# Kernel tuning notes

Hardware: AMD Instinct MI355X
Metric: run time of the kernel (lower is better)

## Reference

```python
import jax, jax.numpy as jnp
import numpy as np
import math

B, S = 4, 1024
V, D, L, H, F, MAXLEN = 32000, 1024, 6, 16, 4096, 2048
DH = D // H
NUM_BUCKETS, MAX_DIST = 32, 256
REL_SCALE = 64.0 ** 0.5
EPS = 1e-5


def setup_inputs() -> dict:
    key = jax.random.key(0)
    ks = iter(jax.random.split(key, 32))
    sd = 0.02
    inp = {
        'src': jax.random.randint(next(ks), (B, S), 0, V),
        'src_mask': jnp.ones((B, 1, 1, S), dtype=jnp.int32),
        'tok_emb': jax.random.normal(next(ks), (V, D), jnp.float32) * sd,
        'pos_emb': jax.random.normal(next(ks), (MAXLEN, D), jnp.float32) * sd,
        'Wq': jax.random.normal(next(ks), (L, D, D), jnp.float32) * sd,
        'bq': jnp.zeros((L, D), jnp.float32),
        'Wk': jax.random.normal(next(ks), (L, D, D), jnp.float32) * sd,
        'bk': jnp.zeros((L, D), jnp.float32),
        'Wv': jax.random.normal(next(ks), (L, D, D), jnp.float32) * sd,
        'bv': jnp.zeros((L, D), jnp.float32),
        'Wo': jax.random.normal(next(ks), (L, D, D), jnp.float32) * sd,
        'bo': jnp.zeros((L, D), jnp.float32),
        'rel_bias': jax.random.normal(next(ks), (L, NUM_BUCKETS, H), jnp.float32) * sd,
        'ln1_g': jnp.ones((L, D), jnp.float32),
        'ln1_b': jnp.zeros((L, D), jnp.float32),
        'W1': jax.random.normal(next(ks), (L, D, F), jnp.float32) * sd,
        'b1': jnp.zeros((L, F), jnp.float32),
        'W2': jax.random.normal(next(ks), (L, F, D), jnp.float32) * sd,
        'b2': jnp.zeros((L, D), jnp.float32),
        'ln2_g': jnp.ones((L, D), jnp.float32),
        'ln2_b': jnp.zeros((L, D), jnp.float32),
    }
    return inp


def _rel_pos_bucket(seq_len):
    # non-causal bucketing (T5-style), matching the torch source
    q = jnp.arange(seq_len)
    k = jnp.arange(seq_len)
    n = q[:, None] - k[None, :]          # == -(k - q)
    nb = NUM_BUCKETS // 2                # 16
    ret = (n < 0).astype(jnp.int32) * nb
    n = jnp.abs(n)
    max_exact = nb // 2                  # 8
    is_small = n < max_exact
    val_large = max_exact + (
        jnp.log(jnp.maximum(n, 1).astype(jnp.float32) / max_exact)
        / math.log(MAX_DIST / max_exact) * (nb - max_exact)
    ).astype(jnp.int32)
    val_large = jnp.minimum(val_large, nb - 1)
    return ret + jnp.where(is_small, n, val_large)  # [S,S] in [0,32)


def _layer_norm(x, g, b):
    mu = jnp.mean(x, axis=-1, keepdims=True)
    var = jnp.var(x, axis=-1, keepdims=True)
    return (x - mu) * jax.lax.rsqrt(var + EPS) * g + b


def reference(src, src_mask, tok_emb, pos_emb, Wq, bq, Wk, bk, Wv, bv, Wo, bo,
              rel_bias, ln1_g, ln1_b, W1, b1, W2, b2, ln2_g, ln2_b):
    seq_len = src.shape[1]
    bucket = _rel_pos_bucket(seq_len)                      # [S,S] int
    x = tok_emb[src] * jnp.sqrt(jnp.float32(D)) + pos_emb[jnp.arange(seq_len)][None]
    scale = jnp.sqrt(jnp.float32(DH))
    neg = jnp.float32(-1e10)

    def layer(x, p):
        (wq, bq_, wk, bk_, wv, bv_, wo, bo_, rb, g1, b1_, w1, bb1, w2, bb2, g2, b2_) = p
        Q = (x @ wq + bq_).reshape(B, seq_len, H, DH)
        K = (x @ wk + bk_).reshape(B, seq_len, H, DH)
        Vv = (x @ wv + bv_).reshape(B, seq_len, H, DH)
        energy = jnp.einsum('bqhd,bkhd->bhqk', Q, K) / scale
        energy = jnp.where(src_mask == 0, neg, energy)
        bias = rb[bucket]                                  # [S,S,H]
        energy = energy + jnp.transpose(bias, (2, 0, 1))[None] * REL_SCALE
        attn = jax.nn.softmax(energy, axis=-1)
        o = jnp.einsum('bhqk,bkhd->bqhd', attn, Vv).reshape(B, seq_len, D)
        o = o @ wo + bo_
        x = _layer_norm(x + o, g1, b1_)
        f = jax.nn.relu(x @ w1 + bb1) @ w2 + bb2
        x = _layer_norm(x + f, g2, b2_)
        return x, None

    params = (Wq, bq, Wk, bk, Wv, bv, Wo, bo, rel_bias,
              ln1_g, ln1_b, W1, b1, W2, b2, ln2_g, ln2_b)
    x, _ = jax.lax.scan(layer, x, params)
    return x
```

## Files before the change

kernel.cpp:

```cpp
#include <hip/hip_runtime.h>

#define B_ 4
#define S_ 1024
#define D_ 1024
#define F_ 4096
#define H_ 16
#define L_ 6
#define M_ (B_*S_)

#define LOG2E 1.44269504088896f

typedef unsigned short u16;
typedef __attribute__((ext_vector_type(4))) unsigned short u16x4;
typedef __attribute__((ext_vector_type(8))) short s16x8;
typedef __attribute__((ext_vector_type(8))) __bf16 bf16x8;
typedef __attribute__((ext_vector_type(4))) float f32x4;

typedef const __attribute__((address_space(1))) unsigned int gu32;
typedef __attribute__((address_space(3))) unsigned int su32;

__device__ __forceinline__ u16 f2bf(float f) {
  union { float f; unsigned u; } v; v.f = f;
  unsigned u = v.u;
  return (u16)((u + 0x7fffu + ((u >> 16) & 1u)) >> 16);
}
__device__ __forceinline__ float bf2f(u16 h) {
  union { unsigned u; float f; } v; v.u = (unsigned)h << 16; return v.f;
}

__device__ __forceinline__ f32x4 mfma16(s16x8 a, s16x8 b, f32x4 c) {
  return __builtin_amdgcn_mfma_f32_16x16x32_bf16(
      __builtin_bit_cast(bf16x8, a), __builtin_bit_cast(bf16x8, b), c, 0, 0, 0);
}

__device__ __forceinline__ void gload16(const void* g, void* s) {
  __builtin_amdgcn_global_load_lds((gu32*)g, (su32*)s, 16, 0, 0);
}

template<int OUTMODE>
__device__ __forceinline__ void gemm128_body(
    const u16* __restrict__ A, const u16* __restrict__ Bt,
    const float* __restrict__ b0, const float* __restrict__ b1,
    const float* __restrict__ b2, u16* __restrict__ Ch,
    int N, int K, int kbeg, int kend)
{
  __shared__ __align__(16) u16 As[128 * 64];
  __shared__ __align__(16) u16 Bs[128 * 64];
  const int tid = threadIdx.x, lane = tid & 63, w = tid >> 6;
  const int bm = blockIdx.x * 128, bn = blockIdx.y * 128;
  const int wm = (w >> 1) * 64, wn = (w & 1) * 64;

  f32x4 acc[4][4];
#pragma unroll
  for (int i = 0; i < 4; i++)
#pragma unroll
    for (int j = 0; j < 4; j++) acc[i][j] = {0.f, 0.f, 0.f, 0.f};

  for (int k0 = kbeg; k0 < kend; k0 += 64) {
    __syncthreads();
#pragma unroll
    for (int i = 0; i < 4; i++) {
      const int flat = i * 4096 + w * 1024 + lane * 16;
      const int row = flat >> 7, ce = (flat & 127) >> 1;
      gload16(A + (size_t)(bm + row) * K + k0 + ce, As + i * 2048 + w * 512);
      gload16(Bt + (size_t)(bn + row) * K + k0 + ce, Bs + i * 2048 + w * 512);
    }
    __syncthreads();
#pragma unroll
    for (int kk = 0; kk < 2; kk++) {
      s16x8 af[4], bf[4];
#pragma unroll
      for (int mf = 0; mf < 4; mf++)
        af[mf] = *(const s16x8*)&As[(wm + mf * 16 + (lane & 15)) * 64 + kk * 32 + (lane >> 4) * 8];
#pragma unroll
      for (int nf = 0; nf < 4; nf++)
        bf[nf] = *(const s16x8*)&Bs[(wn + nf * 16 + (lane & 15)) * 64 + kk * 32 + (lane >> 4) * 8];
#pragma unroll
      for (int mf = 0; mf < 4; mf++)
#pragma unroll
        for (int nf = 0; nf < 4; nf++)
          acc[mf][nf] = mfma16(af[mf], bf[nf], acc[mf][nf]);
    }
  }
#pragma unroll
  for (int nf = 0; nf < 4; nf++) {
    const int col = bn + wn + nf * 16 + (lane & 15);
    float bvv = 0.f, sc = 1.0f;
    int zz = 0, lc = col;
    if (OUTMODE == 3) {
      zz = col >> 10; lc = col & 1023;
      const float* bp = (zz == 0) ? b0 : (zz == 1) ? b1 : b2;
      bvv = bp[lc];
      sc = (zz == 0) ? (0.125f * LOG2E) : 1.0f;
    }
#pragma unroll
    for (int mf = 0; mf < 4; mf++) {
#pragma unroll
      for (int j = 0; j < 4; j++) {
        const int row = bm + wm + mf * 16 + ((lane >> 4) << 2) + j;
        const float v = acc[mf][nf][j];
        if (OUTMODE == 1) {
          Ch[(size_t)row * N + col] = f2bf(v);
        } else {
          Ch[(size_t)zz * M_ * D_ + (size_t)row * D_ + lc] = f2bf((v + bvv) * sc);
        }
      }
    }
  }
}

__global__ __launch_bounds__(256, 3) void gemm_qkvf(
    const u16* __restrict__ A, const u16* __restrict__ WT,
    const float* __restrict__ bq, const float* __restrict__ bk,
    const float* __restrict__ bv, u16* __restrict__ Out)
{
  gemm128_body<3>(A, WT, bq, bk, bv, Out, 3 * D_, D_, 0, D_);
}

__global__ __launch_bounds__(256, 3) void gemm_osplit2(
    const u16* __restrict__ A, const u16* __restrict__ WT,
    u16* __restrict__ P)
{
  const int z = blockIdx.z;
  gemm128_body<1>(A, WT, nullptr, nullptr, nullptr,
                  P + (size_t)z * M_ * D_, D_, D_, z * 512, z * 512 + 512);
}

__device__ __forceinline__ s16x8 readfrag(const u16* half, int r, int kk, int hi4) {
  const int c = (kk * 64 + hi4 * 16) ^ ((r & 7) << 4);
  return *(const s16x8*)((const char*)half + r * 128 + c);
}

__device__ __forceinline__ void stage_half(
    const u16* __restrict__ src, int ldk, u16* lds_half, int w, int lane)
{
#pragma unroll
  for (int j = 0; j < 2; j++) {
    const int flat = j * 8192 + w * 1024 + lane * 16;
    const int row = flat >> 7;
    const int kb = (flat & 127) ^ ((row & 7) << 4);
    gload16(src + (size_t)row * ldk + (kb >> 1), lds_half + j * 4096 + w * 512);
  }
}

#define BAR     asm volatile("s_barrier" ::: "memory")
#define PH_PRE  asm volatile("s_barrier" ::: "memory"); __builtin_amdgcn_s_setprio(1)
#define PH_POST __builtin_amdgcn_s_setprio(0); __builtin_amdgcn_sched_barrier(0)
#define VM4     asm volatile("s_waitcnt vmcnt(4)" ::: "memory")
#define VM0     asm volatile("s_waitcnt vmcnt(0)" ::: "memory")

#define READ_B(bufhalf) do { \
  _Pragma("unroll") for (int nf = 0; nf < 4; nf++) \
  _Pragma("unroll") for (int kk = 0; kk < 2; kk++) \
    bfr[nf][kk] = readfrag(bufhalf, rb0 + nf * 16 + lo16, kk, hi4); } while (0)
#define READ_A(bufhalf, Q) do { \
  _Pragma("unroll") for (int m = 0; m < 2; m++) \
  _Pragma("unroll") for (int kk = 0; kk < 2; kk++) \
    af[m][kk] = readfrag(bufhalf, (2 * (Q) + m) * 16 + lo16, kk, hi4); } while (0)
#define DO_MFMA(Q) do { \
  _Pragma("unroll") for (int kk = 0; kk < 2; kk++) \
  _Pragma("unroll") for (int m = 0; m < 2; m++) \
  _Pragma("unroll") for (int nf = 0; nf < 4; nf++) \
    acc[2 * (Q) + m][nf] = mfma16(af[m][kk], bfr[nf][kk], acc[2 * (Q) + m][nf]); } while (0)

template<int OUTMODE>
__device__ __forceinline__ void gemm256_body(
    const u16* __restrict__ A, const u16* __restrict__ Bt,
    const float* __restrict__ bias, u16* __restrict__ Ch,
    int N, int K, int kbeg, int kslice)
{
  __shared__ __align__(16) u16 As[2][2][8192];
  __shared__ __align__(16) u16 Bs[2][2][8192];
  const int tid = threadIdx.x, lane = tid & 63, w = tid >> 6;
  const int wr = w >> 2, wc = w & 3;
  const int lo16 = lane & 15, hi4 = lane >> 4;
  const int bm = blockIdx.x * 256, bn = blockIdx.y * 256;
  const int rb0 = (wc & 1) * 64;

  const u16* Abase = A + (size_t)bm * K + kbeg;
  const u16* Bbase = Bt + (size_t)bn * K + kbeg;
  const size_t h1 = (size_t)128 * K;
  const int NT = kslice >> 6, NI = NT >> 1;

  f32x4 acc[8][4];
#pragma unroll
  for (int i = 0; i < 8; i++)
#pragma unroll
    for (int j = 0; j < 4; j++) acc[i][j] = {0.f, 0.f, 0.f, 0.f};

  stage_half(Abase,           K, As[0][0], w, lane);
  stage_half(Abase + h1,      K, As[0][1], w, lane);
  stage_half(Bbase,           K, Bs[0][0], w, lane);
  stage_half(Bbase + h1,      K, Bs[0][1], w, lane);
  stage_half(Abase + 64,      K, As[1][0], w, lane);
  stage_half(Abase + h1 + 64, K, As[1][1], w, lane);
  stage_half(Bbase + 64,      K, Bs[1][0], w, lane);
  stage_half(Bbase + h1 + 64, K, Bs[1][1], w, lane);
  asm volatile("s_waitcnt vmcnt(8)" ::: "memory");
  BAR;

  const u16* Ae = As[0][wr]; const u16* Ao = As[1][wr];
  const u16* Be = Bs[0][wc >> 1]; const u16* Bo = Bs[1][wc >> 1];
  s16x8 af[2][2], bfr[4][2];

  for (int it = 0; it < NI - 1; ++it) {
    READ_B(Be); READ_A(Ae, 0);
    if (it > 0) {
      stage_half(Abase +      (size_t)(2 * it + 1) * 64, K, As[1][0], w, lane);
      stage_half(Abase + h1 + (size_t)(2 * it + 1) * 64, K, As[1][1], w, lane);
    }
    PH_PRE; DO_MFMA(0); PH_POST; BAR;
    READ_A(Ae, 1);
    stage_half(Bbase +      (size_t)(2 * it + 2) * 64, K, Bs[0][0], w, lane);
    PH_PRE; DO_MFMA(1); PH_POST; BAR;
    READ_A(Ae, 2);
    stage_half(Bbase + h1 + (size_t)(2 * it + 2) * 64, K, Bs[0][1], w, lane);
    PH_PRE; DO_MFMA(2); PH_POST; BAR;
    READ_A(Ae, 3);
    PH_PRE; DO_MFMA(3); PH_POST; VM4; BAR;
    READ_B(Bo); READ_A(Ao, 0);
    stage_half(Abase +      (size_t)(2 * it + 2) * 64, K, As[0][0], w, lane);
    stage_half(Abase + h1 + (size_t)(2 * it + 2) * 64, K, As[0][1], w, lane);
    PH_PRE; DO_MFMA(0); PH_POST; BAR;
    READ_A(Ao, 1);
    stage_half(Bbase +      (size_t)(2 * it + 3) * 64, K, Bs[1][0], w, lane);
    PH_PRE; DO_MFMA(1); PH_POST; BAR;
    READ_A(Ao, 2);
    stage_half(Bbase + h1 + (size_t)(2 * it + 3) * 64, K, Bs[1][1], w, lane);
    PH_PRE; DO_MFMA(2); PH_POST; BAR;
    READ_A(Ao, 3);
    PH_PRE; DO_MFMA(3); PH_POST; VM4; BAR;
  }
  READ_B(Be); READ_A(Ae, 0);
  stage_half(Abase +      (size_t)(NT - 1) * 64, K, As[1][0], w, lane);
  stage_half(Abase + h1 + (size_t)(NT - 1) * 64, K, As[1][1], w, lane);
  PH_PRE; DO_MFMA(0); PH_POST; BAR;
  READ_A(Ae, 1);             PH_PRE; DO_MFMA(1); PH_POST; BAR;
  READ_A(Ae, 2);             PH_PRE; DO_MFMA(2); PH_POST; BAR;
  READ_A(Ae, 3);             PH_PRE; DO_MFMA(3); PH_POST; VM0; BAR;
  READ_B(Bo); READ_A(Ao, 0); PH_PRE; DO_MFMA(0); PH_POST; BAR;
  READ_A(Ao, 1);             PH_PRE; DO_MFMA(1); PH_POST; BAR;
  READ_A(Ao, 2);             PH_PRE; DO_MFMA(2); PH_POST; BAR;
  READ_A(Ao, 3);             PH_PRE; DO_MFMA(3); PH_POST;

  const int row0 = bm + wr * 128, col0 = bn + wc * 64;
#pragma unroll
  for (int nf = 0; nf < 4; nf++) {
    const int col = col0 + nf * 16 + lo16;
    const float bv = (OUTMODE == 2) ? bias[col] : 0.f;
#pragma unroll
    for (int mf = 0; mf < 8; mf++) {
#pragma unroll
      for (int j = 0; j < 4; j++) {
        const int row = row0 + mf * 16 + hi4 * 4 + j;
        float v = acc[mf][nf][j];
        if (OUTMODE == 2) v = fmaxf(v + bv, 0.f);
        Ch[(size_t)row * N + col] = f2bf(v);
      }
    }
  }
}

__global__ __launch_bounds__(512, 2) void gemm_ffn1(
    const u16* __restrict__ A, const u16* __restrict__ WT,
    const float* __restrict__ bias, u16* __restrict__ Out)
{
  gemm256_body<2>(A, WT, bias, Out, F_, D_, 0, D_);
}

__global__ __launch_bounds__(512, 2) void gemm_ffn2sp4(
    const u16* __restrict__ A, const u16* __restrict__ WT,
    u16* __restrict__ P)
{
  const int z = blockIdx.z;
  gemm256_body<4>(A, WT, nullptr, P + (size_t)z * M_ * D_,
                  D_, F_, z * 1024, 1024);
}

__global__ __launch_bounds__(256) void transpose_all(
    const float* __restrict__ Wq, const float* __restrict__ Wk,
    const float* __restrict__ Wv, const float* __restrict__ Wo,
    const float* __restrict__ W1, const float* __restrict__ W2,
    u16* __restrict__ WTall)
{
  __shared__ float t[32][33];
  const int l = blockIdx.y;
  int bt = blockIdx.x;
  const float* src;
  u16* dst;
  int R, C, cx, cy;
  u16* base = WTall + (size_t)l * 12 * 1024 * 1024;
  if (bt < 4096) {
    const int m = bt >> 10; bt &= 1023;
    src = ((m == 0) ? Wq : (m == 1) ? Wk : (m == 2) ? Wv : Wo) + (size_t)l * D_ * D_;
    dst = base + (size_t)m * D_ * D_;
    R = D_; C = D_; cx = bt & 31; cy = bt >> 5;
  } else if (bt < 8192) {
    bt -= 4096;
    src = W1 + (size_t)l * D_ * F_;
    dst = base + 4 * 1024 * 1024;
    R = D_; C = F_; cx = bt & 127; cy = bt >> 7;
  } else {
    bt -= 8192;
    src = W2 + (size_t)l * D_ * F_;
    dst = base + 8 * 1024 * 1024;
    R = F_; C = D_; cx = bt & 31; cy = bt >> 5;
  }
  const int c0 = cx * 32, r0 = cy * 32;
  const int tx = threadIdx.x & 31, ty = threadIdx.x >> 5;
#pragma unroll
  for (int i = 0; i < 4; i++)
    t[ty + 8 * i][tx] = src[(size_t)(r0 + ty + 8 * i) * C + c0 + tx];
  __syncthreads();
#pragma unroll
  for (int i = 0; i < 4; i++)
    dst[(size_t)(c0 + ty + 8 * i) * R + r0 + tx] = f2bf(t[tx][ty + 8 * i]);
}

__global__ __launch_bounds__(256) void vt_transpose(
    const u16* __restrict__ Vb, u16* __restrict__ Vt)
{
  __shared__ u16 t[64][66];
  const int s0 = blockIdx.x * 64;
  const int bh = blockIdx.y;
  const int b = bh >> 4, h = bh & 15;
  const int tid = threadIdx.x;
  const int row = tid >> 2;
  const int c0 = (tid & 3) * 16;
  const u16* src = Vb + (size_t)(b * S_ + s0 + row) * D_ + h * 64 + c0;
  *(s16x8*)&t[row][c0] = *(const s16x8*)src;
  *(s16x8*)&t[row][c0 + 8] = *(const s16x8*)(src + 8);
  __syncthreads();
  const int dh = tid >> 2;
  const int sc = (tid & 3) * 16;
  s16x8 a, bv;
#pragma unroll
  for (int u = 0; u < 8; u++) a[u] = (short)t[sc + u][dh];
#pragma unroll
  for (int u = 0; u < 8; u++) bv[u] = (short)t[sc + 8 + u][dh];
  u16* dst = Vt + (size_t)(bh * 64 + dh) * S_ + s0 + sc;
  *(s16x8*)dst = a;
  *(s16x8*)(dst + 8) = bv;
}

__global__ __launch_bounds__(256) void build_lut(
    const float* __restrict__ rb, float* __restrict__ lut_g)
{
  const int h = blockIdx.x, l = blockIdx.y;
  for (int idx = threadIdx.x; idx < 2048; idx += 256) {
    const int rel = idx - 1024;
    const int ret = rel < 0 ? 16 : 0;
    const int n = rel < 0 ? -rel : rel;
    int bu;
    if (n < 8) bu = ret + n;
    else {
      const float t = logf((float)n * 0.125f) * (8.0f / 3.4657359027997265f);
      int vl = 8 + (int)t;
      if (vl > 15) vl = 15;
      bu = ret + vl;
    }
    lut_g[(size_t)(l * H_ + h) * 2048 + idx] = rb[l * 512 + bu * 16 + h] * (8.0f * LOG2E);
  }
}

__global__ __launch_bounds__(256) void mask2neg(
    const int* __restrict__ mask, u16* __restrict__ mf)
{
  const int i = blockIdx.x * 256 + threadIdx.x;
  if (i < B_ * S_) mf[i] = mask[i] ? (u16)0 : f2bf(-1e10f * LOG2E);
}

__device__ __forceinline__ s16x8 lds_swz(const u16* base, int row, int cb) {
  const int addr = row * 128 + (cb ^ ((row & 7) << 4));
  return *(const s16x8*)((const char*)base + addr);
}

#define ATTN_STAGE(t, buf) do { \
  const int kt2 = (t) * 64; \
  const int flat2 = tid * 16; \
  const int row2 = flat2 >> 7; \
  const int ce2 = ((flat2 & 127) ^ ((row2 & 7) << 4)) >> 1; \
  gload16(Kb + (size_t)(bS + kt2 + row2) * D_ + hh + ce2, Ks[buf] + w * 512); \
  gload16(Vt + (size_t)(bh * 64 + row2) * S_ + kt2 + ce2, Vs[buf] + w * 512); \
} while (0)

__global__ __launch_bounds__(512, 2) void attn_kernel(
    const u16* __restrict__ Qb, const u16* __restrict__ Kb,
    const u16* __restrict__ Vt, const u16* __restrict__ mask16,
    const float* __restrict__ lut_g, u16* __restrict__ AO)
{
  __shared__ __align__(16) float lut[2048];
  __shared__ __align__(16) u16 maskf[1024];
  __shared__ __align__(16) u16 Ks[2][64 * 64];
  __shared__ __align__(16) u16 Vs[2][64 * 64];
  __shared__ __align__(16) u16 Ps[8][16 * 68];

  const int tid = threadIdx.x;
  const int lane = tid & 63;
  const int w = tid >> 6;
  const int bh = blockIdx.x;
  const int b = bh >> 4, h = bh & 15;
  const int q0 = blockIdx.y * 128 + w * 16;
  const int bS = b * S_, hh = h * 64;
  const int lo16 = lane & 15, hi4 = lane >> 4;

  const float* lsrc = lut_g + (size_t)h * 2048;
  gload16(lsrc + w * 256 + lane * 4, lut + w * 256);
  if (w < 2)
    gload16(mask16 + bS + w * 512 + lane * 8, maskf + w * 512);

  s16x8 qf[2];
#pragma unroll
  for (int kk = 0; kk < 2; kk++)
    qf[kk] = *(const s16x8*)(Qb + (size_t)(bS + q0 + lo16) * D_ + hh +
                             kk * 32 + hi4 * 8);

  s16x8 onesf;
#pragma unroll
  for (int u = 0; u < 8; u++) onesf[u] = (short)((lo16 == 0) ? 0x3F80 : 0);

  f32x4 oacc[5];
#pragma unroll
  for (int i = 0; i < 5; i++) oacc[i] = {0.f, 0.f, 0.f, 0.f};

  ATTN_STAGE(0, 0);
  asm volatile("s_waitcnt vmcnt(0) lgkmcnt(0)" ::: "memory");
  __builtin_amdgcn_s_barrier();

  for (int t = 0; t < S_ / 64; ++t) {
    const int cur = t & 1;
    const int kt = t * 64;
    if (t < S_ / 64 - 1) ATTN_STAGE(t + 1, cur ^ 1);

    f32x4 sacc[4];
#pragma unroll
    for (int i = 0; i < 4; i++) sacc[i] = {0.f, 0.f, 0.f, 0.f};
#pragma unroll
    for (int kk = 0; kk < 2; kk++) {
      const int cb = kk * 64 + hi4 * 16;
#pragma unroll
      for (int nf = 0; nf < 4; nf++) {
        const s16x8 kb = lds_swz(Ks[cur], nf * 16 + lo16, cb);
        sacc[nf] = mfma16(qf[kk], kb, sacc[nf]);
      }
    }

    float kmf[4];
#pragma unroll
    for (int nf = 0; nf < 4; nf++)
      kmf[nf] = bf2f(maskf[kt + nf * 16 + lo16]);

    const int lidx0 = q0 + hi4 * 4 + 1024 - kt - lo16;
#pragma unroll
    for (int j = 0; j < 4; j++) {
      const int lrow = (hi4 << 2) + j;
#pragma unroll
      for (int nf = 0; nf < 4; nf++) {
        const float s = sacc[nf][j] + kmf[nf] + lut[lidx0 + j - nf * 16];
        Ps[w][lrow * 68 + nf * 16 + lo16] = f2bf(__builtin_amdgcn_exp2f(s));
      }
    }

#pragma unroll
    for (int kk = 0; kk < 2; kk++) {
      const s16x8 pa = *(const s16x8*)&Ps[w][lo16 * 68 + kk * 32 + hi4 * 8];
      const int cb = kk * 64 + hi4 * 16;
#pragma unroll
      for (int df = 0; df < 4; df++) {
        const s16x8 vb = lds_swz(Vs[cur], df * 16 + lo16, cb);
        oacc[df] = mfma16(pa, vb, oacc[df]);
      }
      oacc[4] = mfma16(pa, onesf, oacc[4]);
    }

    asm volatile("s_waitcnt vmcnt(0)" ::: "memory");
    __builtin_amdgcn_s_barrier();
  }

  float inv[4];
#pragma unroll
  for (int j = 0; j < 4; j++) {
    const float l = __shfl(oacc[4][j], lane & 48);
    inv[j] = 1.0f / l;
  }
#pragma unroll
  for (int df = 0; df < 4; df++)
#pragma unroll
    for (int j = 0; j < 4; j++) {
      const int qrow = q0 + (hi4 << 2) + j;
      AO[(size_t)(bS + qrow) * D_ + hh + df * 16 + lo16] =
          f2bf(oacc[df][j] * inv[j]);
    }
}

template<int NP>
__global__ __launch_bounds__(256) void ln_fusedb(
    const u16* __restrict__ Xh, const u16* __restrict__ P,
    const float* __restrict__ bias, const float* __restrict__ g,
    const float* __restrict__ be, u16* __restrict__ Yh, float* __restrict__ Yf)
{
  const int row = blockIdx.x;
  const int tid = threadIdx.x;
  const size_t off = (size_t)row * D_;
  const size_t ps = (size_t)M_ * D_;
  const u16x4 xv = ((const u16x4*)(Xh + off))[tid];
  float v[4];
#pragma unroll
  for (int q = 0; q < 4; q++) v[q] = bf2f(xv[q]);
#pragma unroll
  for (int p = 0; p < NP; p++) {
    const u16x4 pv = ((const u16x4*)(P + p * ps + off))[tid];
#pragma unroll
    for (int q = 0; q < 4; q++) v[q] += bf2f(pv[q]);
  }
  const float4 bb = ((const float4*)bias)[tid];
  v[0] += bb.x; v[1] += bb.y; v[2] += bb.z; v[3] += bb.w;

  float sum = v[0] + v[1] + v[2] + v[3];
  float ss = v[0] * v[0] + v[1] * v[1] + v[2] * v[2] + v[3] * v[3];
#pragma unroll
  for (int o = 1; o < 64; o <<= 1) {
    sum += __shfl_xor(sum, o);
    ss += __shfl_xor(ss, o);
  }
  __shared__ float s1[4], s2[4];
  if ((tid & 63) == 0) { s1[tid >> 6] = sum; s2[tid >> 6] = ss; }
  __syncthreads();
  sum = s1[0] + s1[1] + s1[2] + s1[3];
  ss = s2[0] + s2[1] + s2[2] + s2[3];
  const float mu = sum * (1.f / D_);
  const float var = ss * (1.f / D_) - mu * mu;
  const float rstd = rsqrtf(var + 1e-5f);
  const float4 gv = ((const float4*)g)[tid];
  const float4 bv = ((const float4*)be)[tid];
  float y[4];
  y[0] = (v[0] - mu) * rstd * gv.x + bv.x;
  y[1] = (v[1] - mu) * rstd * gv.y + bv.y;
  y[2] = (v[2] - mu) * rstd * gv.z + bv.z;
  y[3] = (v[3] - mu) * rstd * gv.w + bv.w;
  u16x4 hv;
  hv.x = f2bf(y[0]); hv.y = f2bf(y[1]); hv.z = f2bf(y[2]); hv.w = f2bf(y[3]);
  ((u16x4*)(Yh + off))[tid] = hv;
  if (Yf != nullptr) {
    float4 yf; yf.x = y[0]; yf.y = y[1]; yf.z = y[2]; yf.w = y[3];
    ((float4*)(Yf + off))[tid] = yf;
  }
}

__global__ __launch_bounds__(256) void embed_kernel(
    const int* __restrict__ src, const float* __restrict__ tok,
    const float* __restrict__ pos, u16* __restrict__ Xh)
{
  const int row = blockIdx.x;
  const int s = row & (S_ - 1);
  const int t = src[row];
  const int tid = threadIdx.x;
  const float4 tv = ((const float4*)(tok + (size_t)t * D_))[tid];
  const float4 pv = ((const float4*)(pos + (size_t)s * D_))[tid];
  u16x4 hv;
  hv.x = f2bf(tv.x * 32.f + pv.x);
  hv.y = f2bf(tv.y * 32.f + pv.y);
  hv.z = f2bf(tv.z * 32.f + pv.z);
  hv.w = f2bf(tv.w * 32.f + pv.w);
  ((u16x4*)(Xh + (size_t)row * D_))[tid] = hv;
}

extern "C" void kernel_launch(void* const* d_in, const int* in_sizes, int n_in,
                              void* d_out, int out_size, void* d_ws, size_t ws_size,
                              hipStream_t stream)
{
  const int* src = (const int*)d_in[0];
  const int* mask = (const int*)d_in[1];
  const float* tok_emb = (const float*)d_in[2];
  const float* pos_emb = (const float*)d_in[3];
  const float* Wq = (const float*)d_in[4];
  const float* bq = (const float*)d_in[5];
  const float* Wk = (const float*)d_in[6];
  const float* bk = (const float*)d_in[7];
  const float* Wv = (const float*)d_in[8];
  const float* bv = (const float*)d_in[9];
  const float* Wo = (const float*)d_in[10];
  const float* bo = (const float*)d_in[11];
  const float* rb = (const float*)d_in[12];
  const float* g1 = (const float*)d_in[13];
  const float* b1n = (const float*)d_in[14];
  const float* W1 = (const float*)d_in[15];
  const float* b1f = (const float*)d_in[16];
  const float* W2 = (const float*)d_in[17];
  const float* b2f = (const float*)d_in[18];
  const float* g2 = (const float*)d_in[19];
  const float* b2n = (const float*)d_in[20];
  float* out = (float*)d_out;

  char* ws = (char*)d_ws;
  const size_t MB = 1ull << 20;
  u16* xb16  = (u16*)(ws + 0);
  u16* Qb16  = (u16*)(ws + 8 * MB);
  u16* Kb16  = (u16*)(ws + 16 * MB);
  u16* Vb16  = (u16*)(ws + 24 * MB);
  u16* Vt16  = (u16*)(ws + 32 * MB);
  u16* AO16  = (u16*)(ws + 40 * MB);
  u16* Pp16  = (u16*)(ws + 48 * MB);
  u16* WTall = (u16*)(ws + 80 * MB);
  u16* Hb16  = (u16*)(ws + 8 * MB);
  float* lut_g  = (float*)(ws + 224 * MB);
  u16*   mask16 = (u16*)(ws + 224 * MB + 786432);

  embed_kernel<<<M_, 256, 0, stream>>>(src, tok_emb, pos_emb, xb16);
  build_lut<<<dim3(H_, L_), 256, 0, stream>>>(rb, lut_g);
  mask2neg<<<(B_ * S_ + 255) / 256, 256, 0, stream>>>(mask, mask16);
  transpose_all<<<dim3(12288, L_), 256, 0, stream>>>(
      Wq, Wk, Wv, Wo, W1, W2, WTall);

  for (int l = 0; l < L_; l++) {
    u16* WTqkv = WTall + (size_t)l * 12 * 1024 * 1024;
    u16* WTo   = WTqkv + 3 * 1024 * 1024;
    u16* WT1   = WTqkv + 4 * 1024 * 1024;
    u16* WT2   = WTqkv + 8 * 1024 * 1024;

    gemm_qkvf<<<dim3(M_ / 128, 3 * D_ / 128), 256, 0, stream>>>(
        xb16, WTqkv, bq + l * D_, bk + l * D_, bv + l * D_, Qb16);

    vt_transpose<<<dim3(S_ / 64, B_ * H_), 256, 0, stream>>>(Vb16, Vt16);

    attn_kernel<<<dim3(B_ * H_, S_ / 128), 512, 0, stream>>>(
        Qb16, Kb16, Vt16, mask16, lut_g + (size_t)l * H_ * 2048, AO16);

    gemm_osplit2<<<dim3(M_ / 128, D_ / 128, 2), 256, 0, stream>>>(
        AO16, WTo, Pp16);

    ln_fusedb<2><<<M_, 256, 0, stream>>>(
        xb16, Pp16, bo + l * D_, g1 + l * D_, b1n + l * D_, xb16, nullptr);

    gemm_ffn1<<<dim3(M_ / 256, F_ / 256), 512, 0, stream>>>(
        xb16, WT1, b1f + l * F_, Hb16);

    gemm_ffn2sp4<<<dim3(M_ / 256, D_ / 256, 4), 512, 0, stream>>>(
        Hb16, WT2, Pp16);

    ln_fusedb<4><<<M_, 256, 0, stream>>>(
        xb16, Pp16, b2f + l * D_, g2 + l * D_, b2n + l * D_, xb16,
        (l == L_ - 1) ? out : nullptr);
  }
}
```

Before: 1.350 ms.

## Fuse V transpose into QKV GEMM epilogue and transpose weights per layer

The QKV GEMM epilogue now writes V directly in the transposed per-head layout, so the separate vt_transpose kernel and its extra read/write pass over V go away. The one-shot transpose of all layers' weights is replaced by a per-layer transpose kernel that reuses a single bf16 weight buffer. That kernel uses 64x64 tiles with float4 loads and 16-byte stores. The per-layer version shrinks workspace use and may keep weights warmer in cache, at the cost of an extra launch per layer. The transposed V stores are 8-byte strided writes, which may coalesce less well.

Measured after the change: 1.239 ms. 1.09x faster.

```diff
diff --git a/kernel.cpp b/kernel.cpp
--- a/kernel.cpp
+++ b/kernel.cpp
@@ -42,7 +42,7 @@
     const u16* __restrict__ A, const u16* __restrict__ Bt,
     const float* __restrict__ b0, const float* __restrict__ b1,
     const float* __restrict__ b2, u16* __restrict__ Ch,
-    int N, int K, int kbeg, int kend)
+    u16* __restrict__ Vt, int N, int K, int kbeg, int kend)
 {
   __shared__ __align__(16) u16 As[128 * 64];
   __shared__ __align__(16) u16 Bs[128 * 64];
@@ -82,27 +82,55 @@
           acc[mf][nf] = mfma16(af[mf], bf[nf], acc[mf][nf]);
     }
   }
-#pragma unroll
-  for (int nf = 0; nf < 4; nf++) {
-    const int col = bn + wn + nf * 16 + (lane & 15);
-    float bvv = 0.f, sc = 1.0f;
-    int zz = 0, lc = col;
-    if (OUTMODE == 3) {
-      zz = col >> 10; lc = col & 1023;
-      const float* bp = (zz == 0) ? b0 : (zz == 1) ? b1 : b2;
-      bvv = bp[lc];
-      sc = (zz == 0) ? (0.125f * LOG2E) : 1.0f;
-    }
-#pragma unroll
-    for (int mf = 0; mf < 4; mf++) {
-#pragma unroll
-      for (int j = 0; j < 4; j++) {
-        const int row = bm + wm + mf * 16 + ((lane >> 4) << 2) + j;
-        const float v = acc[mf][nf][j];
-        if (OUTMODE == 1) {
-          Ch[(size_t)row * N + col] = f2bf(v);
-        } else {
-          Ch[(size_t)zz * M_ * D_ + (size_t)row * D_ + lc] = f2bf((v + bvv) * sc);
+
+  if (OUTMODE == 3) {
+    const int zz = bn >> 10;
+    const int lcb = (bn & 1023) + wn;
+    const float* bp = (zz == 0) ? b0 : (zz == 1) ? b1 : b2;
+    if (zz == 2) {
+      const int b = bm >> 10;
+#pragma unroll
+      for (int nf = 0; nf < 4; nf++) {
+        const int dh2 = lcb + nf * 16 + (lane & 15);
+        const int hq = dh2 >> 6, dh = dh2 & 63;
+        const float bv = bp[dh2];
+        u16* vrow = Vt + ((size_t)((b << 4) + hq) * 64 + dh) * S_;
+#pragma unroll
+        for (int mf = 0; mf < 4; mf++) {
+          const int s0 = (bm & 1023) + wm + mf * 16 + ((lane >> 4) << 2);
+          u16x4 hv;
+#pragma unroll
+          for (int j = 0; j < 4; j++) hv[j] = f2bf(acc[mf][nf][j] + bv);
+          *(u16x4*)(vrow + s0) = hv;
+        }
+      }
+    } else {
+      const float sc = (zz == 0) ? (0.125f * LOG2E) : 1.0f;
+      u16* Outz = Ch + (size_t)zz * M_ * D_;
+#pragma unroll
+      for (int nf = 0; nf < 4; nf++) {
+        const int col = lcb + nf * 16 + (lane & 15);
+        const float bv = bp[col];
+#pragma unroll
+        for (int mf = 0; mf < 4; mf++) {
+#pragma unroll
+          for (int j = 0; j < 4; j++) {
+            const int row = bm + wm + mf * 16 + ((lane >> 4) << 2) + j;
+            Outz[(size_t)row * D_ + col] = f2bf((acc[mf][nf][j] + bv) * sc);
+          }
+        }
+      }
+    }
+  } else {
+#pragma unroll
+    for (int nf = 0; nf < 4; nf++) {
+      const int col = bn + wn + nf * 16 + (lane & 15);
+#pragma unroll
+      for (int mf = 0; mf < 4; mf++) {
+#pragma unroll
+        for (int j = 0; j < 4; j++) {
+          const int row = bm + wm + mf * 16 + ((lane >> 4) << 2) + j;
+          Ch[(size_t)row * N + col] = f2bf(acc[mf][nf][j]);
         }
       }
     }
@@ -112,9 +140,9 @@
 __global__ __launch_bounds__(256, 3) void gemm_qkvf(
     const u16* __restrict__ A, const u16* __restrict__ WT,
     const float* __restrict__ bq, const float* __restrict__ bk,
-    const float* __restrict__ bv, u16* __restrict__ Out)
-{
-  gemm128_body<3>(A, WT, bq, bk, bv, Out, 3 * D_, D_, 0, D_);
+    const float* __restrict__ bv, u16* __restrict__ Out, u16* __restrict__ Vt)
+{
+  gemm128_body<3>(A, WT, bq, bk, bv, Out, Vt, 3 * D_, D_, 0, D_);
 }
 
 __global__ __launch_bounds__(256, 3) void gemm_osplit2(
@@ -123,7 +151,7 @@
 {
   const int z = blockIdx.z;
   gemm128_body<1>(A, WT, nullptr, nullptr, nullptr,
-                  P + (size_t)z * M_ * D_, D_, D_, z * 512, z * 512 + 512);
+                  P + (size_t)z * M_ * D_, nullptr, D_, D_, z * 512, z * 512 + 512);
 }
 
 __device__ __forceinline__ s16x8 readfrag(const u16* half, int r, int kk, int hi4) {
@@ -277,70 +305,52 @@
                   D_, F_, z * 1024, 1024);
 }
 
-__global__ __launch_bounds__(256) void transpose_all(
+__global__ __launch_bounds__(256) void transpose_layer(
     const float* __restrict__ Wq, const float* __restrict__ Wk,
     const float* __restrict__ Wv, const float* __restrict__ Wo,
     const float* __restrict__ W1, const float* __restrict__ W2,
-    u16* __restrict__ WTall)
-{
-  __shared__ float t[32][33];
-  const int l = blockIdx.y;
+    u16* __restrict__ WT)
+{
+  __shared__ float tl[64][65];
   int bt = blockIdx.x;
-  const float* src;
-  u16* dst;
-  int R, C, cx, cy;
-  u16* base = WTall + (size_t)l * 12 * 1024 * 1024;
-  if (bt < 4096) {
-    const int m = bt >> 10; bt &= 1023;
-    src = ((m == 0) ? Wq : (m == 1) ? Wk : (m == 2) ? Wv : Wo) + (size_t)l * D_ * D_;
-    dst = base + (size_t)m * D_ * D_;
-    R = D_; C = D_; cx = bt & 31; cy = bt >> 5;
-  } else if (bt < 8192) {
-    bt -= 4096;
-    src = W1 + (size_t)l * D_ * F_;
-    dst = base + 4 * 1024 * 1024;
-    R = D_; C = F_; cx = bt & 127; cy = bt >> 7;
+  const float* src; u16* dst; int Rsrc, Csrc, cx, cy;
+  if (bt < 1024) {
+    const int m = bt >> 8; const int t = bt & 255;
+    src = (m == 0) ? Wq : (m == 1) ? Wk : (m == 2) ? Wv : Wo;
+    dst = WT + (size_t)m * 1024 * 1024;
+    Rsrc = 1024; Csrc = 1024; cx = t & 15; cy = t >> 4;
+  } else if (bt < 2048) {
+    const int t = bt - 1024;
+    src = W1; dst = WT + (size_t)4 * 1024 * 1024;
+    Rsrc = 1024; Csrc = 4096; cx = t & 63; cy = t >> 6;
   } else {
-    bt -= 8192;
-    src = W2 + (size_t)l * D_ * F_;
-    dst = base + 8 * 1024 * 1024;
-    R = F_; C = D_; cx = bt & 31; cy = bt >> 5;
-  }
-  const int c0 = cx * 32, r0 = cy * 32;
-  const int tx = threadIdx.x & 31, ty = threadIdx.x >> 5;
-#pragma unroll
-  for (int i = 0; i < 4; i++)
-    t[ty + 8 * i][tx] = src[(size_t)(r0 + ty + 8 * i) * C + c0 + tx];
+    const int t = bt - 2048;
+    src = W2; dst = WT + (size_t)8 * 1024 * 1024;
+    Rsrc = 4096; Csrc = 1024; cx = t & 15; cy = t >> 4;
+  }
+  const int r0 = cy * 64, c0 = cx * 64;
+  const int tid = threadIdx.x;
+  const int rl = tid >> 2, q = tid & 3;
+  const float* sp = src + (size_t)(r0 + rl) * Csrc + c0 + q * 16;
+#pragma unroll
+  for (int i = 0; i < 4; i++) {
+    const float4 v = *(const float4*)(sp + i * 4);
+    tl[rl][q * 16 + i * 4 + 0] = v.x;
+    tl[rl][q * 16 + i * 4 + 1] = v.y;
+    tl[rl][q * 16 + i * 4 + 2] = v.z;
+    tl[rl][q * 16 + i * 4 + 3] = v.w;
+  }
   __syncthreads();
 #pragma unroll
-  for (int i = 0; i < 4; i++)
-    dst[(size_t)(c0 + ty + 8 * i) * R + r0 + tx] = f2bf(t[tx][ty + 8 * i]);
-}
-
-__global__ __launch_bounds__(256) void vt_transpose(
-    const u16* __restrict__ Vb, u16* __restrict__ Vt)
-{
-  __shared__ u16 t[64][66];
-  const int s0 = blockIdx.x * 64;
-  const int bh = blockIdx.y;
-  const int b = bh >> 4, h = bh & 15;
-  const int tid = threadIdx.x;
-  const int row = tid >> 2;
-  const int c0 = (tid & 3) * 16;
-  const u16* src = Vb + (size_t)(b * S_ + s0 + row) * D_ + h * 64 + c0;
-  *(s16x8*)&t[row][c0] = *(const s16x8*)src;
-  *(s16x8*)&t[row][c0 + 8] = *(const s16x8*)(src + 8);
-  __syncthreads();
-  const int dh = tid >> 2;
-  const int sc = (tid & 3) * 16;
-  s16x8 a, bv;
-#pragma unroll
-  for (int u = 0; u < 8; u++) a[u] = (short)t[sc + u][dh];
-#pragma unroll
-  for (int u = 0; u < 8; u++) bv[u] = (short)t[sc + 8 + u][dh];
-  u16* dst = Vt + (size_t)(bh * 64 + dh) * S_ + s0 + sc;
-  *(s16x8*)dst = a;
-  *(s16x8*)(dst + 8) = bv;
+  for (int it = 0; it < 2; it++) {
+    const int idx = tid + it * 256;
+    const int cl = idx >> 3, seg = idx & 7;
+    const int rw0 = seg * 8;
+    s16x8 v8;
+#pragma unroll
+    for (int u = 0; u < 8; u++) v8[u] = (short)f2bf(tl[rw0 + u][cl]);
+    *(s16x8*)(dst + (size_t)(c0 + cl) * Rsrc + r0 + rw0) = v8;
+  }
 }
 
 __global__ __launch_bounds__(256) void build_lut(
@@ -597,31 +607,32 @@
   u16* xb16  = (u16*)(ws + 0);
   u16* Qb16  = (u16*)(ws + 8 * MB);
   u16* Kb16  = (u16*)(ws + 16 * MB);
-  u16* Vb16  = (u16*)(ws + 24 * MB);
-  u16* Vt16  = (u16*)(ws + 32 * MB);
-  u16* AO16  = (u16*)(ws + 40 * MB);
-  u16* Pp16  = (u16*)(ws + 48 * MB);
-  u16* WTall = (u16*)(ws + 80 * MB);
+  u16* Vt16  = (u16*)(ws + 24 * MB);
+  u16* AO16  = (u16*)(ws + 32 * MB);
+  u16* Pp16  = (u16*)(ws + 40 * MB);
+  u16* WT    = (u16*)(ws + 72 * MB);
   u16* Hb16  = (u16*)(ws + 8 * MB);
-  float* lut_g  = (float*)(ws + 224 * MB);
-  u16*   mask16 = (u16*)(ws + 224 * MB + 786432);
+  float* lut_g  = (float*)(ws + 96 * MB);
+  u16*   mask16 = (u16*)(ws + 96 * MB + 786432);
+
+  u16* WTqkv = WT;
+  u16* WTo   = WT + (size_t)3 * 1024 * 1024;
+  u16* WT1   = WT + (size_t)4 * 1024 * 1024;
+  u16* WT2   = WT + (size_t)8 * 1024 * 1024;
 
   embed_kernel<<<M_, 256, 0, stream>>>(src, tok_emb, pos_emb, xb16);
   build_lut<<<dim3(H_, L_), 256, 0, stream>>>(rb, lut_g);
   mask2neg<<<(B_ * S_ + 255) / 256, 256, 0, stream>>>(mask, mask16);
-  transpose_all<<<dim3(12288, L_), 256, 0, stream>>>(
-      Wq, Wk, Wv, Wo, W1, W2, WTall);
 
   for (int l = 0; l < L_; l++) {
-    u16* WTqkv = WTall + (size_t)l * 12 * 1024 * 1024;
-    u16* WTo   = WTqkv + 3 * 1024 * 1024;
-    u16* WT1   = WTqkv + 4 * 1024 * 1024;
-    u16* WT2   = WTqkv + 8 * 1024 * 1024;
+    const size_t oDD = (size_t)l * D_ * D_;
+    const size_t oDF = (size_t)l * D_ * F_;
+
+    transpose_layer<<<3072, 256, 0, stream>>>(
+        Wq + oDD, Wk + oDD, Wv + oDD, Wo + oDD, W1 + oDF, W2 + oDF, WT);
 
     gemm_qkvf<<<dim3(M_ / 128, 3 * D_ / 128), 256, 0, stream>>>(
-        xb16, WTqkv, bq + l * D_, bk + l * D_, bv + l * D_, Qb16);
-
-    vt_transpose<<<dim3(S_ / 64, B_ * H_), 256, 0, stream>>>(Vb16, Vt16);
+        xb16, WTqkv, bq + l * D_, bk + l * D_, bv + l * D_, Qb16, Vt16);
 
     attn_kernel<<<dim3(B_ * H_, S_ / 128), 512, 0, stream>>>(
         Qb16, Kb16, Vt16, mask16, lut_g + (size_t)l * H_ * 2048, AO16);
```
